# Kernel tuning notes

Hardware: AMD Instinct MI355X
Metric: run time of the kernel (lower is better)

## Reference

```python
import jax, jax.numpy as jnp
import numpy as np

K = 4096   # infeatures
N = 11008  # outfeatures
T = 8192   # tokens (batch*seq)
GROUP = 32
E8M0_BIAS = 127
E2M1_VALS = jnp.array([0.0, 0.5, 1.0, 1.5, 2.0, 3.0, 4.0, 6.0], dtype=jnp.float32)


def setup_inputs() -> dict:
    key = jax.random.key(0)
    k1, k2, k3, k4 = jax.random.split(key, 4)
    x = jax.random.normal(k1, (T, K), dtype=jnp.float32)
    # packed fp4: 8 nibbles per int32 along the in-feature axis -> [K//8, N]
    weight_packed = jax.random.randint(k2, (K // 8, N), 0, 2147483647, dtype=jnp.int32)
    # e8m0 exponents near the bias so 2^(e-127) stays well-conditioned in fp32
    weight_scale_e8m0 = 112 + jax.random.randint(k3, (K // GROUP, N), 0, 30, dtype=jnp.int32)
    bias = jax.random.normal(k4, (N,), dtype=jnp.float32)
    return {"x": x, "weight_packed": weight_packed,
            "weight_scale_e8m0": weight_scale_e8m0, "bias": bias}


def dequantize_weight(weight_packed, weight_scale_e8m0):
    # unpack 8 fp4 nibbles per int32: nibble j -> in-feature row r*8 + j
    shifts = (jnp.arange(8, dtype=jnp.int32) * 4)[None, :, None]       # [1,8,1]
    nib = (weight_packed[:, None, :] >> shifts) & 0xF                   # [K//8,8,N]
    mag = E2M1_VALS[nib & 0x7]                                           # e2m1 magnitude
    sign = jnp.where((nib >> 3) & 1 == 1, -1.0, 1.0).astype(jnp.float32)
    w = (mag * sign).reshape(K, N)
    # per-group e8m0 scale: 2^(e - 127), groups of 32 along in-features
    scale = jnp.exp2((weight_scale_e8m0 - E8M0_BIAS).astype(jnp.float32))  # [K//32,N]
    w = (w.reshape(K // GROUP, GROUP, N) * scale[:, None, :]).reshape(K, N)
    return w


def reference(x, weight_packed, weight_scale_e8m0, bias):
    w = dequantize_weight(weight_packed, weight_scale_e8m0)  # [K, N]
    return x @ w + bias                                       # [T, N]
```

## Files before the change

### kernel.cpp

```cpp
#include <hip/hip_runtime.h>


#define TDIM 8192
#define KDIM 4096
#define NDIM 11008

typedef __attribute__((ext_vector_type(8))) short short8;
typedef __attribute__((ext_vector_type(8))) unsigned short ushort8;
typedef __attribute__((ext_vector_type(4))) float f32x4;
typedef __attribute__((ext_vector_type(16))) float f32x16;

__device__ __forceinline__ unsigned short f2bf(float f) {
    unsigned int u = __float_as_uint(f);
    u += 0x7FFFu + ((u >> 16) & 1u);
    return (unsigned short)(u >> 16);
}

__device__ __forceinline__ unsigned short nib2bf(unsigned int v, int e) {
    unsigned int m3 = v & 7u;
    if (m3 == 0u) return 0;
    unsigned int s = (v & 8u) << 12;
    unsigned int E = (unsigned int)e + (m3 >> 1) - 1u;
    unsigned int man = (m3 >= 2u) ? ((m3 & 1u) << 6) : 0u;
    return (unsigned short)(s | (E << 7) | man);
}

__device__ __forceinline__ void gload_lds16(const void* g, void* l) {
    __builtin_amdgcn_global_load_lds(
        (const __attribute__((address_space(1))) void*)g,
        (__attribute__((address_space(3))) void*)l, 16, 0, 0);
}

__global__ __launch_bounds__(256) void convert_x(const float* __restrict__ x,
                                                 unsigned short* __restrict__ xbf) {
    size_t i = ((size_t)blockIdx.x * 256 + threadIdx.x) * 8;
    float4 v0 = *(const float4*)(x + i);
    float4 v1 = *(const float4*)(x + i + 4);
    ushort8 r;
    r[0] = f2bf(v0.x); r[1] = f2bf(v0.y); r[2] = f2bf(v0.z); r[3] = f2bf(v0.w);
    r[4] = f2bf(v1.x); r[5] = f2bf(v1.y); r[6] = f2bf(v1.z); r[7] = f2bf(v1.w);
    *(ushort8*)(xbf + i) = r;
}

__global__ __launch_bounds__(256) void dequant_w(const int* __restrict__ wp,
                                                 const int* __restrict__ wse,
                                                 unsigned short* __restrict__ wt) {
    __shared__ int sT[64][65];
    const int tid = threadIdx.x;
    const int n0 = blockIdx.x * 64;
    const int r0 = blockIdx.y * 64;

    #pragma unroll
    for (int i = 0; i < 16; ++i) {
        int idx = i * 256 + tid;
        int r = idx >> 6, n = idx & 63;
        sT[r][n] = wp[(size_t)(r0 + r) * NDIM + n0 + n];
    }
    __syncthreads();
    #pragma unroll
    for (int i = 0; i < 16; ++i) {
        int idx = i * 256 + tid;
        int n = idx >> 6, r = idx & 63;
        unsigned int p = (unsigned int)sT[r][n];
        int e = wse[(size_t)((r0 + r) >> 2) * NDIM + n0 + n];
        ushort8 o;
        #pragma unroll
        for (int j = 0; j < 8; ++j) o[j] = nib2bf((p >> (4 * j)) & 0xFu, e);
        *(ushort8*)(wt + (size_t)(n0 + n) * KDIM + (size_t)(r0 + r) * 8) = o;
    }
}

#define STG(PJ0, PJ1, GOFF, C, MAT, HK)                                        \
    do {                                                                       \
        gload_lds16((PJ0) + (GOFF), ldsW + (C)*32768 + (MAT)*16384 + (HK)*8192);           \
        gload_lds16((PJ1) + (GOFF), ldsW + (C)*32768 + (MAT)*16384 + (HK)*8192 + 4096);    \
    } while (0)

#define RD_A32(CB, KS, MH, DST)                                                                \
    DST[0] = *(const short8*)(ldsC + (CB)*65536 + (KS)*16384 + (((MH)*2+0)*2)*1024 + aoff + ofK0); \
    DST[1] = *(const short8*)(ldsC + (CB)*65536 + (KS)*16384 + (((MH)*2+0)*2)*1024 + aoff + ofK1); \
    DST[2] = *(const short8*)(ldsC + (CB)*65536 + (KS)*16384 + (((MH)*2+1)*2)*1024 + aoff + ofK0); \
    DST[3] = *(const short8*)(ldsC + (CB)*65536 + (KS)*16384 + (((MH)*2+1)*2)*1024 + aoff + ofK1);

#define RD_B32(CB, KS, DST)                                                                    \
    DST[0] = *(const short8*)(ldsC + (CB)*65536 + 32768 + (KS)*16384 + 0*2048 + boff + ofK0);  \
    DST[1] = *(const short8*)(ldsC + (CB)*65536 + 32768 + (KS)*16384 + 0*2048 + boff + ofK1);  \
    DST[2] = *(const short8*)(ldsC + (CB)*65536 + 32768 + (KS)*16384 + 1*2048 + boff + ofK0);  \
    DST[3] = *(const short8*)(ldsC + (CB)*65536 + 32768 + (KS)*16384 + 1*2048 + boff + ofK1);

#define CLUSTER32(A, B, MH)                                                    \
    __builtin_amdgcn_s_setprio(1);                                             \
    _Pragma("unroll")                                                          \
    for (int kk_ = 0; kk_ < 2; ++kk_) {                                        \
        _Pragma("unroll")                                                      \
        for (int m_ = 0; m_ < 2; ++m_) {                                       \
            _Pragma("unroll")                                                  \
            for (int n_ = 0; n_ < 2; ++n_)                                     \
                acc[(MH)*2 + m_][n_] = __builtin_amdgcn_mfma_f32_32x32x16_bf16( \
                    A[m_*2 + kk_], B[n_*2 + kk_], acc[(MH)*2 + m_][n_], 0, 0, 0); \
        }                                                                      \
    }                                                                          \
    __builtin_amdgcn_s_setprio(0);

#define BODY(T, C)                                                             \
    do {                                                                       \
                       \
        if ((T) < 63) STG(pA0, pA1, 96, (C)^1, 0, 1);                          \
        RD_A32((C), 0, 1, aY)                                                  \
        CLUSTER32(aX, bX, 0)                                                   \
                \
        if ((T) < 63) STG(pB0, pB1, 96, (C)^1, 1, 1);                          \
        RD_B32((C), 1, bY)                                                     \
        RD_A32((C), 1, 0, aX)                                                  \
        CLUSTER32(aY, bX, 1)                                                   \
        if ((T) < 63) asm volatile("s_waitcnt vmcnt(4)" ::: "memory");         \
        __builtin_amdgcn_s_barrier();                                          \
              \
        if ((T) < 62) STG(pA0, pA1, 128, (C), 0, 0);                           \
        RD_A32((C), 1, 1, aY)                                                  \
        CLUSTER32(aX, bY, 0)                                                   \
                       \
        if ((T) < 62) STG(pB0, pB1, 128, (C), 1, 0);                           \
        if ((T) < 63) { RD_B32((C)^1, 0, bX) RD_A32((C)^1, 0, 0, aX) }         \
        CLUSTER32(aY, bY, 1)                                                   \
        if ((T) < 62)       asm volatile("s_waitcnt vmcnt(4)" ::: "memory");   \
        else if ((T) == 62) asm volatile("s_waitcnt vmcnt(0)" ::: "memory");   \
        __builtin_amdgcn_s_barrier();                                          \
        pA0 += 64; pA1 += 64; pB0 += 64; pB1 += 64;                            \
    } while (0)

__global__ __launch_bounds__(512, 1) void gemm256(const unsigned short* __restrict__ xbf,
                                                  const unsigned short* __restrict__ wt,
                                                  const float* __restrict__ bias,
                                                  float* __restrict__ out) {
    __shared__ __attribute__((aligned(16))) unsigned short lds[2][2][16384];
    const int tid = threadIdx.x;
    const int l = tid & 63, wid = tid >> 6;
    const int wm = wid >> 2, wn = wid & 3;

    int b = blockIdx.x;
    int swz = (b & 7) * 172 + (b >> 3);
    int band = swz / 344;
    int r = swz % 344;
    int st = r >> 5; if (st > 10) st = 10;
    int ii = r - (st << 5);
    int w = (st < 10) ? 4 : 3;
    const int bm0 = (band * 8 + ii / w) * 256;
    const int bn0 = (st * 4 + ii % w) * 256;

    int rs0, ks0, rs1, ks1;
    {
        int chunk = wid * 64 + l;
        int cin = chunk & 63;
        cin ^= ((cin >> 5) & 1) << 1;
        rs0 = (chunk >> 6) * 16 + (cin >> 2);
        ks0 = (cin & 3) * 8;
        chunk = 512 + wid * 64 + l;
        cin = chunk & 63;
        cin ^= ((cin >> 5) & 1) << 1;
        rs1 = (chunk >> 6) * 16 + (cin >> 2);
        ks1 = (cin & 3) * 8;
    }

    const unsigned short* pA0 = xbf + (size_t)(bm0 + rs0) * KDIM + ks0;
    const unsigned short* pA1 = xbf + (size_t)(bm0 + rs1) * KDIM + ks1;
    const unsigned short* pB0 = wt + (size_t)(bn0 + rs0) * KDIM + ks0;
    const unsigned short* pB1 = wt + (size_t)(bn0 + rs1) * KDIM + ks1;

    unsigned short* ldsW = &lds[0][0][0] + wid * 512;
    const char* ldsC = (const char*)&lds[0][0][0];

    const int s3 = (l >> 3) & 1;
    const int lbase = ((l >> 4) & 1) * 1024 + (l & 15) * 64 + ((l >> 5) << 4);
    const int ofK0 = lbase + (s3 << 5);
    const int ofK1 = lbase + ((s3 ^ 1) << 5);
    const int aoff = wm * 8192;
    const int boff = wn * 4096;

    f32x16 acc[4][2] = {};
    short8 aX[4], aY[4], bX[4], bY[4];

    STG(pA0, pA1, 0, 0, 0, 0);
    STG(pB0, pB1, 0, 0, 1, 0);
    STG(pA0, pA1, 32, 0, 0, 1);
    STG(pB0, pB1, 32, 0, 1, 1);
    STG(pA0, pA1, 64, 1, 0, 0);
    STG(pB0, pB1, 64, 1, 1, 0);
    asm volatile("s_waitcnt vmcnt(4)" ::: "memory");
    __builtin_amdgcn_s_barrier();
    RD_B32(0, 0, bX)
    RD_A32(0, 0, 0, aX)

    for (int tt = 0; tt < 32; ++tt) {
        BODY(2 * tt, 0);
        BODY(2 * tt + 1, 1);
    }

    const int ecol = l & 31, erow = (l >> 5) * 4;
    #pragma unroll
    for (int nb = 0; nb < 2; ++nb) {
        int col = bn0 + wn * 64 + nb * 32 + ecol;
        float bv = bias[col];
        #pragma unroll
        for (int mb = 0; mb < 4; ++mb) {
            int rowbase = bm0 + wm * 128 + mb * 32 + erow;
            #pragma unroll
            for (int reg = 0; reg < 16; ++reg) {
                int row = rowbase + (reg & 3) + 8 * (reg >> 2);
                __builtin_nontemporal_store(acc[mb][nb][reg] + bv,
                                            &out[(size_t)row * NDIM + col]);
            }
        }
    }
}

__global__ __launch_bounds__(256, 2) void gemm_fused(const float* __restrict__ x,
                                                     const int* __restrict__ wp,
                                                     const int* __restrict__ wse,
                                                     const float* __restrict__ bias,
                                                     float* __restrict__ out) {
    __shared__ __attribute__((aligned(16))) unsigned short lA[128 * 64];
    __shared__ __attribute__((aligned(16))) unsigned short lB[128 * 64];
    const int tid = threadIdx.x;
    const int l = tid & 63, wid = tid >> 6;
    const int bn0 = blockIdx.x * 128, bm0 = blockIdx.y * 128;
    const int wm = wid >> 1, wn = wid & 1;

    f32x4 acc[4][4] = {};

    for (int k0 = 0; k0 < KDIM; k0 += 64) {
        float4 av0[4], av1[4];
        unsigned int bp[4];
        int be[4];
        #pragma unroll
        for (int i = 0; i < 4; ++i) {
            int seg = i * 256 + tid;
            int row = seg >> 3, kseg = seg & 7;
            const float4* p = (const float4*)(x + (size_t)(bm0 + row) * KDIM + k0 + kseg * 8);
            av0[i] = p[0]; av1[i] = p[1];
        }
        #pragma unroll
        for (int i = 0; i < 4; ++i) {
            int idx = i * 256 + tid;
            int ln = idx & 127, lr = idx >> 7;
            bp[i] = ((const unsigned int*)wp)[(size_t)(k0 / 8 + lr) * NDIM + bn0 + ln];
            be[i] = wse[(size_t)((k0 + lr * 8) >> 5) * NDIM + bn0 + ln];
        }
        #pragma unroll
        for (int i = 0; i < 4; ++i) {
            int seg = i * 256 + tid;
            int row = seg >> 3, kseg = seg & 7;
            ushort8 r;
            r[0] = f2bf(av0[i].x); r[1] = f2bf(av0[i].y); r[2] = f2bf(av0[i].z); r[3] = f2bf(av0[i].w);
            r[4] = f2bf(av1[i].x); r[5] = f2bf(av1[i].y); r[6] = f2bf(av1[i].z); r[7] = f2bf(av1[i].w);
            *(ushort8*)&lA[row * 64 + kseg * 8] = r;
        }
        #pragma unroll
        for (int i = 0; i < 4; ++i) {
            int idx = i * 256 + tid;
            int ln = idx & 127, lr = idx >> 7;
            unsigned int p = bp[i];
            int e = be[i];
            ushort8 r;
            #pragma unroll
            for (int j = 0; j < 8; ++j) r[j] = nib2bf((p >> (4 * j)) & 0xFu, e);
            *(ushort8*)&lB[ln * 64 + lr * 8] = r;
        }
        __syncthreads();
        #pragma unroll
        for (int kc = 0; kc < 2; ++kc) {
            short8 a[4], bb[4];
            #pragma unroll
            for (int f = 0; f < 4; ++f) {
                a[f] = *(const short8*)&lA[(wm * 64 + f * 16 + (l & 15)) * 64 + kc * 32 + (l >> 4) * 8];
                bb[f] = *(const short8*)&lB[(wn * 64 + f * 16 + (l & 15)) * 64 + kc * 32 + (l >> 4) * 8];
            }
            #pragma unroll
            for (int fm = 0; fm < 4; ++fm)
                #pragma unroll
                for (int fn = 0; fn < 4; ++fn)
                    acc[fm][fn] = __builtin_amdgcn_mfma_f32_16x16x32_bf16(a[fm], bb[fn], acc[fm][fn], 0, 0, 0);
        }
        __syncthreads();
    }

    const int crow = (l >> 4) * 4, ccol = l & 15;
    #pragma unroll
    for (int fn = 0; fn < 4; ++fn) {
        int col = bn0 + wn * 64 + fn * 16 + ccol;
        float bv = bias[col];
        #pragma unroll
        for (int fm = 0; fm < 4; ++fm) {
            int row0 = bm0 + wm * 64 + fm * 16 + crow;
            #pragma unroll
            for (int j = 0; j < 4; ++j)
                out[(size_t)(row0 + j) * NDIM + col] = acc[fm][fn][j] + bv;
        }
    }
}

extern "C" void kernel_launch(void* const* d_in, const int* in_sizes, int n_in,
                              void* d_out, int out_size, void* d_ws, size_t ws_size,
                              hipStream_t stream) {
    (void)in_sizes; (void)n_in; (void)out_size;
    const float* x = (const float*)d_in[0];
    const int* wp = (const int*)d_in[1];
    const int* wse = (const int*)d_in[2];
    const float* bias = (const float*)d_in[3];
    float* out = (float*)d_out;

    const size_t xbf_bytes = (size_t)TDIM * KDIM * 2;
    const size_t wt_bytes = (size_t)NDIM * KDIM * 2;

    if (ws_size >= xbf_bytes + wt_bytes) {
        unsigned short* xbf = (unsigned short*)d_ws;
        unsigned short* wt = (unsigned short*)((char*)d_ws + xbf_bytes);
        hipLaunchKernelGGL(convert_x, dim3((TDIM * KDIM) / (256 * 8)), dim3(256), 0, stream, x, xbf);
        hipLaunchKernelGGL(dequant_w, dim3(NDIM / 64, (KDIM / 8) / 64), dim3(256), 0, stream, wp, wse, wt);
        hipLaunchKernelGGL(gemm256, dim3((NDIM / 256) * (TDIM / 256)), dim3(512), 0, stream, xbf, wt, bias, out);
    } else {
        hipLaunchKernelGGL(gemm_fused, dim3(NDIM / 128, TDIM / 128), dim3(256), 0, stream, x, wp, wse, bias, out);
    }
}
```

Baseline: 734.8 us.

## Restructure LDS tile layout to 16-wide k-slices with simpler loads and reads

Changes the global-to-LDS staging so each thread loads two adjacent 16-byte chunks from one row, dropping the XOR-swizzled dual-row mapping. The LDS tile is reorganized into four 16-element k sub-slices per 32-k chunk, and the MFMA clusters now consume one k-slice over all four M blocks per step instead of splitting M halves across two k steps. The aim is fewer address registers and simpler LDS read offsets. Without the swizzle, LDS reads with a 32-byte row stride may hit more bank conflicts, and the global loads cover less contiguous memory per wave.

```diff
diff --git a/kernel.cpp b/kernel.cpp
--- a/kernel.cpp
+++ b/kernel.cpp
@@ -70,63 +70,61 @@
     }
 }
 
-#define STG(PJ0, PJ1, GOFF, C, MAT, HK)                                        \
+#define STG(P, GOFF, C, MAT, HK)                                               \
     do {                                                                       \
-        gload_lds16((PJ0) + (GOFF), ldsW + (C)*32768 + (MAT)*16384 + (HK)*8192);           \
-        gload_lds16((PJ1) + (GOFF), ldsW + (C)*32768 + (MAT)*16384 + (HK)*8192 + 4096);    \
+        gload_lds16((P) + (GOFF), ldsW + (C)*32768 + (MAT)*16384 + (HK)*8192);            \
+        gload_lds16((P) + (GOFF) + 16, ldsW + (C)*32768 + (MAT)*16384 + (HK)*8192 + 4096); \
     } while (0)
 
-#define RD_A32(CB, KS, MH, DST)                                                                \
-    DST[0] = *(const short8*)(ldsC + (CB)*65536 + (KS)*16384 + (((MH)*2+0)*2)*1024 + aoff + ofK0); \
-    DST[1] = *(const short8*)(ldsC + (CB)*65536 + (KS)*16384 + (((MH)*2+0)*2)*1024 + aoff + ofK1); \
-    DST[2] = *(const short8*)(ldsC + (CB)*65536 + (KS)*16384 + (((MH)*2+1)*2)*1024 + aoff + ofK0); \
-    DST[3] = *(const short8*)(ldsC + (CB)*65536 + (KS)*16384 + (((MH)*2+1)*2)*1024 + aoff + ofK1);
-
-#define RD_B32(CB, KS, DST)                                                                    \
-    DST[0] = *(const short8*)(ldsC + (CB)*65536 + 32768 + (KS)*16384 + 0*2048 + boff + ofK0);  \
-    DST[1] = *(const short8*)(ldsC + (CB)*65536 + 32768 + (KS)*16384 + 0*2048 + boff + ofK1);  \
-    DST[2] = *(const short8*)(ldsC + (CB)*65536 + 32768 + (KS)*16384 + 1*2048 + boff + ofK0);  \
-    DST[3] = *(const short8*)(ldsC + (CB)*65536 + 32768 + (KS)*16384 + 1*2048 + boff + ofK1);
-
-#define CLUSTER32(A, B, MH)                                                    \
+#define RD_A32(CB, S, DST)                                                                         \
+    DST[0] = *(const short8*)(ldsC + (CB)*65536 + ((S)>>1)*16384 + ((S)&1)*8192 + aoff + 0*1024 + rdoff); \
+    DST[1] = *(const short8*)(ldsC + (CB)*65536 + ((S)>>1)*16384 + ((S)&1)*8192 + aoff + 1*1024 + rdoff); \
+    DST[2] = *(const short8*)(ldsC + (CB)*65536 + ((S)>>1)*16384 + ((S)&1)*8192 + aoff + 2*1024 + rdoff); \
+    DST[3] = *(const short8*)(ldsC + (CB)*65536 + ((S)>>1)*16384 + ((S)&1)*8192 + aoff + 3*1024 + rdoff);
+
+#define RD_B32(CB, S, DST)                                                                         \
+    DST[0] = *(const short8*)(ldsC + (CB)*65536 + 32768 + ((S)>>1)*16384 + ((S)&1)*8192 + boff + 0*1024 + rdoff); \
+    DST[1] = *(const short8*)(ldsC + (CB)*65536 + 32768 + ((S)>>1)*16384 + ((S)&1)*8192 + boff + 1*1024 + rdoff);
+
+#define CLUSTER32(A, B)                                                        \
     __builtin_amdgcn_s_setprio(1);                                             \
     _Pragma("unroll")                                                          \
-    for (int kk_ = 0; kk_ < 2; ++kk_) {                                        \
+    for (int m_ = 0; m_ < 4; ++m_) {                                           \
         _Pragma("unroll")                                                      \
-        for (int m_ = 0; m_ < 2; ++m_) {                                       \
-            _Pragma("unroll")                                                  \
-            for (int n_ = 0; n_ < 2; ++n_)                                     \
-                acc[(MH)*2 + m_][n_] = __builtin_amdgcn_mfma_f32_32x32x16_bf16( \
-                    A[m_*2 + kk_], B[n_*2 + kk_], acc[(MH)*2 + m_][n_], 0, 0, 0); \
-        }                                                                      \
+        for (int n_ = 0; n_ < 2; ++n_)                                         \
+            acc[m_][n_] = __builtin_amdgcn_mfma_f32_32x32x16_bf16(             \
+                A[m_], B[n_], acc[m_][n_], 0, 0, 0);                           \
     }                                                                          \
     __builtin_amdgcn_s_setprio(0);
 
 #define BODY(T, C)                                                             \
     do {                                                                       \
-                       \
-        if ((T) < 63) STG(pA0, pA1, 96, (C)^1, 0, 1);                          \
-        RD_A32((C), 0, 1, aY)                                                  \
-        CLUSTER32(aX, bX, 0)                                                   \
-                \
-        if ((T) < 63) STG(pB0, pB1, 96, (C)^1, 1, 1);                          \
+                     \
+        if ((T) < 63) STG(pA, 96, (C)^1, 0, 1);                                \
+        RD_A32((C), 1, aY)                                                     \
         RD_B32((C), 1, bY)                                                     \
-        RD_A32((C), 1, 0, aX)                                                  \
-        CLUSTER32(aY, bX, 1)                                                   \
+        CLUSTER32(aX, bX)                                                      \
+                     \
+        if ((T) < 63) STG(pB, 96, (C)^1, 1, 1);                                \
+        RD_A32((C), 2, aX)                                                     \
+        RD_B32((C), 2, bX)                                                     \
+        CLUSTER32(aY, bY)                                                      \
+        \
         if ((T) < 63) asm volatile("s_waitcnt vmcnt(4)" ::: "memory");         \
         __builtin_amdgcn_s_barrier();                                          \
-              \
-        if ((T) < 62) STG(pA0, pA1, 128, (C), 0, 0);                           \
-        RD_A32((C), 1, 1, aY)                                                  \
-        CLUSTER32(aX, bY, 0)                                                   \
-                       \
-        if ((T) < 62) STG(pB0, pB1, 128, (C), 1, 0);                           \
-        if ((T) < 63) { RD_B32((C)^1, 0, bX) RD_A32((C)^1, 0, 0, aX) }         \
-        CLUSTER32(aY, bY, 1)                                                   \
+                \
+        if ((T) < 62) STG(pA, 128, (C), 0, 0);                                 \
+        RD_A32((C), 3, aY)                                                     \
+        RD_B32((C), 3, bY)                                                     \
+        CLUSTER32(aX, bX)                                                      \
+                         \
+        if ((T) < 62) STG(pB, 128, (C), 1, 0);                                 \
+        if ((T) < 63) { RD_A32((C)^1, 0, aX) RD_B32((C)^1, 0, bX) }            \
+        CLUSTER32(aY, bY)                                                      \
         if ((T) < 62)       asm volatile("s_waitcnt vmcnt(4)" ::: "memory");   \
         else if ((T) == 62) asm volatile("s_waitcnt vmcnt(0)" ::: "memory");   \
         __builtin_amdgcn_s_barrier();                                          \
-        pA0 += 64; pA1 += 64; pB0 += 64; pB1 += 64;                            \
+        pA += 64; pB += 64;                                                    \
     } while (0)
 
 __global__ __launch_bounds__(512, 1) void gemm256(const unsigned short* __restrict__ xbf,
@@ -148,48 +146,32 @@
     const int bm0 = (band * 8 + ii / w) * 256;
     const int bn0 = (st * 4 + ii % w) * 256;
 
-    int rs0, ks0, rs1, ks1;
-    {
-        int chunk = wid * 64 + l;
-        int cin = chunk & 63;
-        cin ^= ((cin >> 5) & 1) << 1;
-        rs0 = (chunk >> 6) * 16 + (cin >> 2);
-        ks0 = (cin & 3) * 8;
-        chunk = 512 + wid * 64 + l;
-        cin = chunk & 63;
-        cin ^= ((cin >> 5) & 1) << 1;
-        rs1 = (chunk >> 6) * 16 + (cin >> 2);
-        ks1 = (cin & 3) * 8;
-    }
-
-    const unsigned short* pA0 = xbf + (size_t)(bm0 + rs0) * KDIM + ks0;
-    const unsigned short* pA1 = xbf + (size_t)(bm0 + rs1) * KDIM + ks1;
-    const unsigned short* pB0 = wt + (size_t)(bn0 + rs0) * KDIM + ks0;
-    const unsigned short* pB1 = wt + (size_t)(bn0 + rs1) * KDIM + ks1;
+    const int rs = wid * 32 + (l >> 1);
+    const int ks = (l & 1) * 8;
+
+    const unsigned short* pA = xbf + (size_t)(bm0 + rs) * KDIM + ks;
+    const unsigned short* pB = wt + (size_t)(bn0 + rs) * KDIM + ks;
 
     unsigned short* ldsW = &lds[0][0][0] + wid * 512;
     const char* ldsC = (const char*)&lds[0][0][0];
 
-    const int s3 = (l >> 3) & 1;
-    const int lbase = ((l >> 4) & 1) * 1024 + (l & 15) * 64 + ((l >> 5) << 4);
-    const int ofK0 = lbase + (s3 << 5);
-    const int ofK1 = lbase + ((s3 ^ 1) << 5);
-    const int aoff = wm * 8192;
-    const int boff = wn * 4096;
+    const int rdoff = (l & 31) * 32 + ((l >> 5) << 4);
+    const int aoff = wm * 4096;
+    const int boff = wn * 2048;
 
     f32x16 acc[4][2] = {};
-    short8 aX[4], aY[4], bX[4], bY[4];
-
-    STG(pA0, pA1, 0, 0, 0, 0);
-    STG(pB0, pB1, 0, 0, 1, 0);
-    STG(pA0, pA1, 32, 0, 0, 1);
-    STG(pB0, pB1, 32, 0, 1, 1);
-    STG(pA0, pA1, 64, 1, 0, 0);
-    STG(pB0, pB1, 64, 1, 1, 0);
+    short8 aX[4], aY[4], bX[2], bY[2];
+
+    STG(pA, 0, 0, 0, 0);
+    STG(pB, 0, 0, 1, 0);
+    STG(pA, 32, 0, 0, 1);
+    STG(pB, 32, 0, 1, 1);
+    STG(pA, 64, 1, 0, 0);
+    STG(pB, 64, 1, 1, 0);
     asm volatile("s_waitcnt vmcnt(4)" ::: "memory");
     __builtin_amdgcn_s_barrier();
+    RD_A32(0, 0, aX)
     RD_B32(0, 0, bX)
-    RD_A32(0, 0, 0, aX)
 
     for (int tt = 0; tt < 32; ++tt) {
         BODY(2 * tt, 0);
```

After: 764.4 us. +4.0%, slower.
